# Optimization experiments

Measured on AMD Instinct MI355X. Metric: run time of the kernel, lower is better.

Reference implementation:

```python
import jax, jax.numpy as jnp
import numpy as np

EPS_COS = 1e-8   # torch cosine_similarity eps
EPS_LN = 1e-5    # torch LayerNorm eps
SLOPE = 0.01     # torch LeakyReLU default negative_slope
N_HOP = 3
D_MODEL = 512
TEMP = 10.0


def _cos_sim(q, s):
    # q: [B, D], s: [B, S, D] -> [B, S]
    dot = jnp.einsum('bd,bsd->bs', q, s)
    qn = jnp.linalg.norm(q, axis=-1)          # [B]
    sn = jnp.linalg.norm(s, axis=-1)          # [B, S]
    return dot / jnp.maximum(qn[:, None] * sn, EPS_COS)


def _layer_norm(x, gamma, beta):
    mu = jnp.mean(x, axis=-1, keepdims=True)
    var = jnp.mean(jnp.square(x - mu), axis=-1, keepdims=True)
    return (x - mu) * jax.lax.rsqrt(var + EPS_LN) * gamma + beta


def setup_inputs() -> dict:
    key = jax.random.key(0)
    k1, k2, k3, k4 = jax.random.split(key, 4)
    B, S, D = 256, 512, D_MODEL
    query_emb = jax.random.normal(k1, (B, D), dtype=jnp.float32)
    state_emb = jax.random.normal(k2, (B, S, D), dtype=jnp.float32)
    # Stacked per-hop Linear params (txt branch), kaiming-uniform-ish scale
    lim = 1.0 / np.sqrt(D)
    W = jax.random.uniform(k3, (N_HOP, D, D), jnp.float32, -lim, lim)
    b = jax.random.uniform(k4, (N_HOP, D), jnp.float32, -lim, lim)
    ln_gamma = jnp.ones((D,), jnp.float32)
    ln_beta = jnp.zeros((D,), jnp.float32)
    return {"query_emb": query_emb, "state_emb": state_emb, "W": W, "b": b,
            "ln_gamma": ln_gamma, "ln_beta": ln_beta}


def reference(query_emb, state_emb, W, b, ln_gamma, ln_beta):
    q, s = query_emb, state_emb
    for i in range(N_HOP):
        dist = jax.nn.softmax(_cos_sim(q, s) * TEMP, axis=-1)       # [B, S]
        s = jax.nn.leaky_relu(jnp.einsum('bsd,de->bse', s, W[i].T) + b[i],
                              negative_slope=SLOPE)                  # [B, S, D]
        agg = jnp.einsum('bs,bsd->bd', dist, s)                      # [B, D]
        q = _layer_norm(q + agg, ln_gamma, ln_beta)
    final_dist = jax.nn.softmax(_cos_sim(q, s) * TEMP, axis=-1)
    return (q, final_dist)
```

## Files before the change

### kernel.cpp

```cpp
#include <hip/hip_runtime.h>
#include <hip/hip_bf16.h>
#include <stdint.h>

#define D 512
#define BATCH 256
#define SEQ 512

typedef __attribute__((ext_vector_type(8))) short short8;
typedef __attribute__((ext_vector_type(4))) float floatx4;

__device__ __forceinline__ float bf2f(unsigned short u) {
    union { unsigned int i; float f; } x; x.i = ((unsigned int)u) << 16; return x.f;
}
__device__ __forceinline__ unsigned short f2bf(float f) {
    union { float f; unsigned int i; } x; x.f = f;
    unsigned int i = x.i;
    unsigned int lsb = (i >> 16) & 1u;
    i += 0x7fffu + lsb;
    return (unsigned short)(i >> 16);
}

__device__ __forceinline__ float wred_sum(float v) {
    #pragma unroll
    for (int o = 32; o; o >>= 1) v += __shfl_xor(v, o, 64);
    return v;
}

__device__ __forceinline__ void llds16(const void* g, void* l) {
    auto gp = (const __attribute__((address_space(1))) void*)(g);
    auto lp = (__attribute__((address_space(3))) void*)(uintptr_t)(l);
    __builtin_amdgcn_global_load_lds(gp, lp, 16, 0, 0);
}

#define FENCE() asm volatile("" ::: "memory")
#define BARRIER() do { FENCE(); __builtin_amdgcn_s_barrier(); FENCE(); } while (0)

template<int WN>
__device__ __forceinline__ void waitvm() {
    if constexpr (WN == 6)      asm volatile("s_waitcnt vmcnt(6)" ::: "memory");
    else if constexpr (WN == 4) asm volatile("s_waitcnt vmcnt(4)" ::: "memory");
    else if constexpr (WN == 2) asm volatile("s_waitcnt vmcnt(2)" ::: "memory");
    else if constexpr (WN == 0) asm volatile("s_waitcnt vmcnt(0)" ::: "memory");
}

template<bool F32IN>
__global__ __launch_bounds__(512)
void scores_kernel(const void* __restrict__ s_in_, const float* __restrict__ q,
                   float* __restrict__ dist_out, unsigned short* __restrict__ s_bf_out) {
    const int b = blockIdx.x, t = threadIdx.x, lane = t & 63, w = t >> 6;
    __shared__ float sc[SEQ];
    __shared__ float red[8];
    __shared__ float m_s, sum_s;

    float qv[8];
    {
        const float4* qp = (const float4*)(q + (size_t)b * D + lane * 8);
        float4 a = qp[0], c = qp[1];
        qv[0] = a.x; qv[1] = a.y; qv[2] = a.z; qv[3] = a.w;
        qv[4] = c.x; qv[5] = c.y; qv[6] = c.z; qv[7] = c.w;
    }
    float qn2 = 0.f;
    #pragma unroll
    for (int j = 0; j < 8; ++j) qn2 += qv[j] * qv[j];
    const float qn = sqrtf(wred_sum(qn2));

    const size_t bbase = (size_t)b * (SEQ * D);
    for (int j = 0; j < 64; j += 2) {
        const int r0 = w * 64 + j;
        float v0[8], v1[8];
        const size_t off0 = bbase + (size_t)r0 * D + lane * 8;
        const size_t off1 = off0 + D;
        if (F32IN) {
            const float4* p0 = (const float4*)((const float*)s_in_ + off0);
            const float4* p1 = (const float4*)((const float*)s_in_ + off1);
            float4 a0 = p0[0], c0 = p0[1], a1 = p1[0], c1 = p1[1];
            v0[0]=a0.x; v0[1]=a0.y; v0[2]=a0.z; v0[3]=a0.w;
            v0[4]=c0.x; v0[5]=c0.y; v0[6]=c0.z; v0[7]=c0.w;
            v1[0]=a1.x; v1[1]=a1.y; v1[2]=a1.z; v1[3]=a1.w;
            v1[4]=c1.x; v1[5]=c1.y; v1[6]=c1.z; v1[7]=c1.w;
            short8 w0, w1;
            #pragma unroll
            for (int k = 0; k < 8; ++k) { w0[k] = (short)f2bf(v0[k]); w1[k] = (short)f2bf(v1[k]); }
            *(short8*)(s_bf_out + off0) = w0;
            *(short8*)(s_bf_out + off1) = w1;
        } else {
            short8 w0 = *(const short8*)((const unsigned short*)s_in_ + off0);
            short8 w1 = *(const short8*)((const unsigned short*)s_in_ + off1);
            #pragma unroll
            for (int k = 0; k < 8; ++k) { v0[k] = bf2f((unsigned short)w0[k]); v1[k] = bf2f((unsigned short)w1[k]); }
        }
        float d0 = 0.f, n0 = 0.f, d1 = 0.f, n1 = 0.f;
        #pragma unroll
        for (int k = 0; k < 8; ++k) {
            d0 += v0[k] * qv[k]; n0 += v0[k] * v0[k];
            d1 += v1[k] * qv[k]; n1 += v1[k] * v1[k];
        }
        d0 = wred_sum(d0); n0 = wred_sum(n0);
        d1 = wred_sum(d1); n1 = wred_sum(n1);
        if (lane == 0) {
            sc[r0]     = 10.f * d0 / fmaxf(qn * sqrtf(n0), 1e-8f);
            sc[r0 + 1] = 10.f * d1 / fmaxf(qn * sqrtf(n1), 1e-8f);
        }
    }
    __syncthreads();

    const float sv = sc[t];
    float m = sv;
    #pragma unroll
    for (int o = 32; o; o >>= 1) m = fmaxf(m, __shfl_xor(m, o, 64));
    if (lane == 0) red[w] = m;
    __syncthreads();
    if (t == 0) {
        float mm = red[0];
        #pragma unroll
        for (int k = 1; k < 8; ++k) mm = fmaxf(mm, red[k]);
        m_s = mm;
    }
    __syncthreads();
    const float e = __expf(sv - m_s);
    float es = wred_sum(e);
    if (lane == 0) red[w] = es;
    __syncthreads();
    if (t == 0) {
        float s = 0.f;
        #pragma unroll
        for (int k = 0; k < 8; ++k) s += red[k];
        sum_s = s;
    }
    __syncthreads();
    dist_out[b * SEQ + t] = e / sum_s;
}

#define NKT 8

#define STA(BUF, H, KT) { const unsigned short* s_ = pA + (H) * 128 * D + (KT) * 64; \
    llds16(s_, &AsL[BUF][H][t * 8]); llds16(s_ + 64 * D, &AsL[BUF][H][t * 8 + 4096]); }
#define STB(BUF, H, KT) { const unsigned short* s_ = pB + (H) * 128 * D + (KT) * 64; \
    llds16(s_, &BsL[BUF][H][t * 8]); llds16(s_ + 64 * D, &BsL[BUF][H][t * 8 + 4096]); }

#define LDAF(BUF, MH) { _Pragma("unroll") for (int j = 0; j < 4; ++j) { \
    af[j][0] = *(const short8*)&AsL[BUF][MH][aoff[j] + xk0]; \
    af[j][1] = *(const short8*)&AsL[BUF][MH][aoff[j] + xk1]; } }
#define LDBF(BUF, NH) { _Pragma("unroll") for (int i = 0; i < 2; ++i) { \
    bfr[i][0] = *(const short8*)&BsL[BUF][NH][boff[i] + xk0]; \
    bfr[i][1] = *(const short8*)&BsL[BUF][NH][boff[i] + xk1]; } }

#define MMQ(MH, NH) { __builtin_amdgcn_s_setprio(1); \
    _Pragma("unroll") for (int kh = 0; kh < 2; ++kh) \
    _Pragma("unroll") for (int j = 0; j < 4; ++j) \
    _Pragma("unroll") for (int i = 0; i < 2; ++i) \
        acc[(MH) * 4 + j][(NH) * 2 + i] = __builtin_amdgcn_mfma_f32_16x16x32_bf16( \
            af[j][kh], bfr[i][kh], acc[(MH) * 4 + j][(NH) * 2 + i], 0, 0, 0); \
    __builtin_amdgcn_s_setprio(0); }

__global__ __launch_bounds__(512, 2)
void gemm_kernel(const unsigned short* __restrict__ A, const unsigned short* __restrict__ Bt,
                 const float* __restrict__ bias, const float* __restrict__ dist,
                 unsigned short* __restrict__ C, float* __restrict__ part) {
    __shared__ __align__(16) unsigned short AsL[2][2][128 * 64];
    __shared__ __align__(16) unsigned short BsL[2][2][128 * 64];
    __shared__ float dls[256];
    __shared__ float agg_lds[2][256];

    const int t = threadIdx.x, lane = t & 63, wid = t >> 6;
    const int wr = wid >> 2, wc = wid & 3;
    const int rr = lane & 15, lg = lane >> 4;
    const int mB = blockIdx.x >> 1, nB = blockIdx.x & 1;
    const size_t tileM = (size_t)mB * 256;
    const int tileN = nB * 256;

    float b_r[4];
    #pragma unroll
    for (int ni = 0; ni < 4; ++ni) b_r[ni] = bias[tileN + (ni * 4 + wc) * 16 + rr];

    if (t < 128) {
        float2 v = *(const float2*)&dist[tileM + 2 * t];
        dls[2 * t] = v.x; dls[2 * t + 1] = v.y;
    }
    asm volatile("s_waitcnt lgkmcnt(0)" ::: "memory");

    const int srow = t >> 3, gc = (t & 7) ^ (srow & 7);
    const unsigned short* pA = A + (tileM + srow) * D + gc * 8;
    const unsigned short* pB = Bt + (size_t)(tileN + srow) * D + gc * 8;

    int aoff[4], boff[2];
    #pragma unroll
    for (int j = 0; j < 4; ++j) aoff[j] = ((j * 2 + wr) * 16 + rr) * 64;
    #pragma unroll
    for (int i = 0; i < 2; ++i) boff[i] = ((i * 4 + wc) * 16 + rr) * 64;
    const int xk0 = ((lg) ^ (rr & 7)) * 8;
    const int xk1 = ((4 + lg) ^ (rr & 7)) * 8;

    floatx4 acc[8][4];
    #pragma unroll
    for (int i = 0; i < 8; ++i)
        #pragma unroll
        for (int j = 0; j < 4; ++j) acc[i][j] = {0.f, 0.f, 0.f, 0.f};

    short8 af[4][2], bfr[2][2];

    STA(0, 0, 0); STB(0, 0, 0); STB(0, 1, 0); STA(0, 1, 0);

    for (int kt = 0; kt < NKT - 1; ++kt) {
        const int rb = kt & 1, sb = rb ^ 1, nk = kt + 1;
        STA(sb, 0, nk); waitvm<6>(); BARRIER();
        LDAF(rb, 0); LDBF(rb, 0); MMQ(0, 0); BARRIER();
        STB(sb, 0, nk); waitvm<6>(); BARRIER();
        LDBF(rb, 1); MMQ(0, 1); BARRIER();
        STB(sb, 1, nk); waitvm<6>(); BARRIER();
        LDAF(rb, 1); LDBF(rb, 0); MMQ(1, 0); BARRIER();
        STA(sb, 1, nk); BARRIER();
        LDBF(rb, 1); MMQ(1, 1); BARRIER();
    }
    {
        waitvm<4>(); BARRIER();
        LDAF(1, 0); LDBF(1, 0); MMQ(0, 0); BARRIER();
        waitvm<2>(); BARRIER();
        LDBF(1, 1); MMQ(0, 1); BARRIER();
        waitvm<0>(); BARRIER();
        LDAF(1, 1); LDBF(1, 0); MMQ(1, 0); BARRIER();
        LDBF(1, 1); MMQ(1, 1);
    }
    __syncthreads();

    float pacc[4] = {0.f, 0.f, 0.f, 0.f};
    #pragma unroll
    for (int mi = 0; mi < 8; ++mi) {
        const int rowb = (mi * 2 + wr) * 16 + lg * 4;
        const float4 dv = *(const float4*)&dls[rowb];
        #pragma unroll
        for (int ni = 0; ni < 4; ++ni) {
            const int col = tileN + (ni * 4 + wc) * 16 + rr;
            #pragma unroll
            for (int r2 = 0; r2 < 4; ++r2) {
                float v = acc[mi][ni][r2] + b_r[ni];
                v = v >= 0.f ? v : 0.01f * v;
                C[(tileM + rowb + r2) * D + col] = f2bf(v);
                pacc[ni] += (&dv.x)[r2] * v;
            }
        }
    }
    #pragma unroll
    for (int ni = 0; ni < 4; ++ni) {
        float p = pacc[ni];
        p += __shfl_xor(p, 16, 64);
        p += __shfl_xor(p, 32, 64);
        if (lg == 0) agg_lds[wr][(ni * 4 + wc) * 16 + rr] = p;
    }
    __syncthreads();
    if (t < 256) {
        const int b = mB >> 1;
        const float s = agg_lds[0][t] + agg_lds[1][t];
        part[(size_t)(mB & 1) * (BATCH * D) + (size_t)b * D + tileN + t] = s;
    }
}

__global__ __launch_bounds__(256)
void aggln_kernel(const float* __restrict__ part, const float* __restrict__ q_in,
                  const float* __restrict__ gamma, const float* __restrict__ beta,
                  float* __restrict__ q_out) {
    const int b = blockIdx.x, t = threadIdx.x, lane = t & 63, wv = t >> 6;
    __shared__ float red[8];
    __shared__ float mu_s, rstd_s;

    const int c0 = 2 * t;
    float2 v0 = *(const float2*)(part + (size_t)b * D + c0);
    float2 v1 = *(const float2*)(part + (size_t)(BATCH * D) + (size_t)b * D + c0);
    float x0 = q_in[b * D + c0] + v0.x + v1.x;
    float x1 = q_in[b * D + c0 + 1] + v0.y + v1.y;

    float sm = wred_sum(x0 + x1);
    if (lane == 0) red[wv] = sm;
    __syncthreads();
    if (t == 0) mu_s = (red[0] + red[1] + red[2] + red[3]) * (1.f / 512.f);
    __syncthreads();
    const float mu = mu_s;
    float d0 = x0 - mu, d1 = x1 - mu;
    float vv = wred_sum(d0 * d0 + d1 * d1);
    if (lane == 0) red[wv] = vv;
    __syncthreads();
    if (t == 0) rstd_s = rsqrtf((red[0] + red[1] + red[2] + red[3]) * (1.f / 512.f) + 1e-5f);
    __syncthreads();
    const float rs = rstd_s;
    q_out[b * D + c0]     = d0 * rs * gamma[c0]     + beta[c0];
    q_out[b * D + c0 + 1] = d1 * rs * gamma[c0 + 1] + beta[c0 + 1];
}

__global__ __launch_bounds__(256)
void convw_kernel(const float* __restrict__ W, unsigned short* __restrict__ Wb, int n4) {
    int i = blockIdx.x * 256 + threadIdx.x;
    if (i < n4) {
        float4 v = *(const float4*)(W + (size_t)i * 4);
        ushort4 o;
        o.x = f2bf(v.x); o.y = f2bf(v.y); o.z = f2bf(v.z); o.w = f2bf(v.w);
        *(ushort4*)(Wb + (size_t)i * 4) = o;
    }
}

extern "C" void kernel_launch(void* const* d_in, const int* in_sizes, int n_in,
                              void* d_out, int out_size, void* d_ws, size_t ws_size,
                              hipStream_t stream) {
    const float* query = (const float*)d_in[0];
    const float* state = (const float*)d_in[1];
    const float* W     = (const float*)d_in[2];
    const float* bias  = (const float*)d_in[3];
    const float* gamma = (const float*)d_in[4];
    const float* beta  = (const float*)d_in[5];

    float* out_q    = (float*)d_out;
    float* out_dist = (float*)d_out + BATCH * SEQ;

    char* ws = (char*)d_ws;
    const size_t SBYTES = (size_t)BATCH * SEQ * D * 2;
    unsigned short* sA = (unsigned short*)ws;
    unsigned short* sB = (unsigned short*)(ws + SBYTES);
    char* ext = ws + 2 * SBYTES;
    float* dist = (float*)ext;
    float* qbuf = (float*)(ext + 524288);
    float* part = (float*)(ext + 2 * 524288);
    unsigned short* Wb = (unsigned short*)(ext + 4 * 524288);

    hipMemcpyAsync(qbuf, query, (size_t)BATCH * D * sizeof(float),
                   hipMemcpyDeviceToDevice, stream);
    convw_kernel<<<768, 256, 0, stream>>>(W, Wb, 3 * D * D / 4);

    dim3 ggrid(BATCH * SEQ / 256 * 2);

    scores_kernel<true><<<BATCH, 512, 0, stream>>>(state, qbuf, dist, sA);
    gemm_kernel<<<ggrid, 512, 0, stream>>>(sA, Wb, bias, dist, sB, part);
    aggln_kernel<<<BATCH, 256, 0, stream>>>(part, qbuf, gamma, beta, qbuf);
    scores_kernel<false><<<BATCH, 512, 0, stream>>>(sB, qbuf, dist, nullptr);
    gemm_kernel<<<ggrid, 512, 0, stream>>>(sB, Wb + D * D, bias + D, dist, sA, part);
    aggln_kernel<<<BATCH, 256, 0, stream>>>(part, qbuf, gamma, beta, qbuf);
    scores_kernel<false><<<BATCH, 512, 0, stream>>>(sA, qbuf, dist, nullptr);
    gemm_kernel<<<ggrid, 512, 0, stream>>>(sA, Wb + 2 * D * D, bias + 2 * D, dist, sB, part);
    aggln_kernel<<<BATCH, 256, 0, stream>>>(part, qbuf, gamma, beta, out_q);
    scores_kernel<false><<<BATCH, 512, 0, stream>>>(sB, out_q, out_dist, nullptr);
}
```

Baseline: 489.8 us.

## Fuse LayerNorm into cosine-score softmax kernel and widen score blocks to 1024 threads

Merges the aggregate+LayerNorm kernel into the following cosine-similarity/softmax kernel, so the updated query is computed in LDS and scored in one launch. It also drops the initial query memcpy by reading the input query directly. Score kernels now use 1024 threads, with 16-lane groups per row covering the full row in 4 strided chunks, which gives more rows in flight and shorter reductions. The trade-off is fewer launches and less q round-tripping against larger blocks with idle half-threads during the softmax phase.

```diff
diff --git a/kernel.cpp b/kernel.cpp
--- a/kernel.cpp
+++ b/kernel.cpp
@@ -25,6 +25,11 @@
     for (int o = 32; o; o >>= 1) v += __shfl_xor(v, o, 64);
     return v;
 }
+__device__ __forceinline__ float gred_sum16(float v) {
+    #pragma unroll
+    for (int o = 8; o; o >>= 1) v += __shfl_xor(v, o, 64);
+    return v;
+}
 
 __device__ __forceinline__ void llds16(const void* g, void* l) {
     auto gp = (const __attribute__((address_space(1))) void*)(g);
@@ -43,72 +48,66 @@
     else if constexpr (WN == 0) asm volatile("s_waitcnt vmcnt(0)" ::: "memory");
 }
 
-template<bool F32IN>
-__global__ __launch_bounds__(512)
-void scores_kernel(const void* __restrict__ s_in_, const float* __restrict__ q,
-                   float* __restrict__ dist_out, unsigned short* __restrict__ s_bf_out) {
+__global__ __launch_bounds__(1024)
+void scores0_kernel(const float* __restrict__ state, const float* __restrict__ query,
+                    float* __restrict__ dist_out, unsigned short* __restrict__ s_bf_out) {
     const int b = blockIdx.x, t = threadIdx.x, lane = t & 63, w = t >> 6;
+    const int g = lane >> 4, ll = lane & 15;
     __shared__ float sc[SEQ];
     __shared__ float red[8];
     __shared__ float m_s, sum_s;
 
-    float qv[8];
+    float qv[4][8];
     {
-        const float4* qp = (const float4*)(q + (size_t)b * D + lane * 8);
-        float4 a = qp[0], c = qp[1];
-        qv[0] = a.x; qv[1] = a.y; qv[2] = a.z; qv[3] = a.w;
-        qv[4] = c.x; qv[5] = c.y; qv[6] = c.z; qv[7] = c.w;
+        const float* qp = query + (size_t)b * D + ll * 8;
+        #pragma unroll
+        for (int j = 0; j < 4; ++j) {
+            float4 a = *(const float4*)(qp + j * 128);
+            float4 c = *(const float4*)(qp + j * 128 + 4);
+            qv[j][0]=a.x; qv[j][1]=a.y; qv[j][2]=a.z; qv[j][3]=a.w;
+            qv[j][4]=c.x; qv[j][5]=c.y; qv[j][6]=c.z; qv[j][7]=c.w;
+        }
     }
     float qn2 = 0.f;
     #pragma unroll
-    for (int j = 0; j < 8; ++j) qn2 += qv[j] * qv[j];
-    const float qn = sqrtf(wred_sum(qn2));
+    for (int j = 0; j < 4; ++j)
+        #pragma unroll
+        for (int e = 0; e < 8; ++e) qn2 += qv[j][e] * qv[j][e];
+    const float qn = sqrtf(gred_sum16(qn2));
 
     const size_t bbase = (size_t)b * (SEQ * D);
-    for (int j = 0; j < 64; j += 2) {
-        const int r0 = w * 64 + j;
-        float v0[8], v1[8];
-        const size_t off0 = bbase + (size_t)r0 * D + lane * 8;
-        const size_t off1 = off0 + D;
-        if (F32IN) {
-            const float4* p0 = (const float4*)((const float*)s_in_ + off0);
-            const float4* p1 = (const float4*)((const float*)s_in_ + off1);
-            float4 a0 = p0[0], c0 = p0[1], a1 = p1[0], c1 = p1[1];
-            v0[0]=a0.x; v0[1]=a0.y; v0[2]=a0.z; v0[3]=a0.w;
-            v0[4]=c0.x; v0[5]=c0.y; v0[6]=c0.z; v0[7]=c0.w;
-            v1[0]=a1.x; v1[1]=a1.y; v1[2]=a1.z; v1[3]=a1.w;
-            v1[4]=c1.x; v1[5]=c1.y; v1[6]=c1.z; v1[7]=c1.w;
-            short8 w0, w1;
+    #pragma unroll 2
+    for (int i = 0; i < 8; ++i) {
+        const int row = w * 32 + i * 4 + g;
+        const float* rp = state + bbase + (size_t)row * D + ll * 8;
+        unsigned short* op = s_bf_out + bbase + (size_t)row * D + ll * 8;
+        float dot = 0.f, nr = 0.f;
+        #pragma unroll
+        for (int j = 0; j < 4; ++j) {
+            float4 a = *(const float4*)(rp + j * 128);
+            float4 c = *(const float4*)(rp + j * 128 + 4);
+            float v[8] = {a.x, a.y, a.z, a.w, c.x, c.y, c.z, c.w};
+            short8 wv;
             #pragma unroll
-            for (int k = 0; k < 8; ++k) { w0[k] = (short)f2bf(v0[k]); w1[k] = (short)f2bf(v1[k]); }
-            *(short8*)(s_bf_out + off0) = w0;
-            *(short8*)(s_bf_out + off1) = w1;
-        } else {
-            short8 w0 = *(const short8*)((const unsigned short*)s_in_ + off0);
-            short8 w1 = *(const short8*)((const unsigned short*)s_in_ + off1);
+            for (int e = 0; e < 8; ++e) wv[e] = (short)f2bf(v[e]);
+            *(short8*)(op + j * 128) = wv;
             #pragma unroll
-            for (int k = 0; k < 8; ++k) { v0[k] = bf2f((unsigned short)w0[k]); v1[k] = bf2f((unsigned short)w1[k]); }
+            for (int e = 0; e < 8; ++e) { dot += v[e] * qv[j][e]; nr += v[e] * v[e]; }
         }
-        float d0 = 0.f, n0 = 0.f, d1 = 0.f, n1 = 0.f;
-        #pragma unroll
-        for (int k = 0; k < 8; ++k) {
-            d0 += v0[k] * qv[k]; n0 += v0[k] * v0[k];
-            d1 += v1[k] * qv[k]; n1 += v1[k] * v1[k];
-        }
-        d0 = wred_sum(d0); n0 = wred_sum(n0);
-        d1 = wred_sum(d1); n1 = wred_sum(n1);
-        if (lane == 0) {
-            sc[r0]     = 10.f * d0 / fmaxf(qn * sqrtf(n0), 1e-8f);
-            sc[r0 + 1] = 10.f * d1 / fmaxf(qn * sqrtf(n1), 1e-8f);
-        }
-    }
-    __syncthreads();
-
-    const float sv = sc[t];
-    float m = sv;
-    #pragma unroll
-    for (int o = 32; o; o >>= 1) m = fmaxf(m, __shfl_xor(m, o, 64));
-    if (lane == 0) red[w] = m;
+        dot = gred_sum16(dot);
+        nr  = gred_sum16(nr);
+        if (ll == 0) sc[row] = 10.f * dot / fmaxf(qn * sqrtf(nr), 1e-8f);
+    }
+    __syncthreads();
+
+    float sv = 0.f, ev = 0.f;
+    if (t < 512) {
+        sv = sc[t];
+        float m = sv;
+        #pragma unroll
+        for (int o = 32; o; o >>= 1) m = fmaxf(m, __shfl_xor(m, o, 64));
+        if (lane == 0) red[w] = m;
+    }
     __syncthreads();
     if (t == 0) {
         float mm = red[0];
@@ -117,9 +116,11 @@
         m_s = mm;
     }
     __syncthreads();
-    const float e = __expf(sv - m_s);
-    float es = wred_sum(e);
-    if (lane == 0) red[w] = es;
+    if (t < 512) {
+        ev = __expf(sv - m_s);
+        float es = wred_sum(ev);
+        if (lane == 0) red[w] = es;
+    }
     __syncthreads();
     if (t == 0) {
         float s = 0.f;
@@ -128,7 +129,111 @@
         sum_s = s;
     }
     __syncthreads();
-    dist_out[b * SEQ + t] = e / sum_s;
+    if (t < 512) dist_out[b * SEQ + t] = ev / sum_s;
+}
+
+__global__ __launch_bounds__(1024)
+void fused_kernel(const unsigned short* __restrict__ S, const float* __restrict__ part,
+                  const float* __restrict__ q_in, const float* __restrict__ gamma,
+                  const float* __restrict__ beta, float* __restrict__ q_out,
+                  float* __restrict__ dist_out) {
+    const int b = blockIdx.x, t = threadIdx.x, lane = t & 63, w = t >> 6;
+    const int g = lane >> 4, ll = lane & 15;
+    __shared__ float qs[D];
+    __shared__ float sc[SEQ];
+    __shared__ float red[8];
+    __shared__ float mu_s, rstd_s, qn_s, m_s, sum_s;
+
+    float x = 0.f;
+    if (t < 512) {
+        const float a = part[(size_t)b * D + t] + part[(size_t)(BATCH * D) + (size_t)b * D + t];
+        x = q_in[(size_t)b * D + t] + a;
+        float sm = wred_sum(x);
+        if (lane == 0) red[w] = sm;
+    }
+    __syncthreads();
+    if (t == 0) mu_s = (red[0]+red[1]+red[2]+red[3]+red[4]+red[5]+red[6]+red[7]) * (1.f / 512.f);
+    __syncthreads();
+    if (t < 512) {
+        const float d = x - mu_s;
+        float vv = wred_sum(d * d);
+        if (lane == 0) red[w] = vv;
+    }
+    __syncthreads();
+    if (t == 0) rstd_s = rsqrtf((red[0]+red[1]+red[2]+red[3]+red[4]+red[5]+red[6]+red[7]) * (1.f / 512.f) + 1e-5f);
+    __syncthreads();
+    if (t < 512) {
+        const float y = (x - mu_s) * rstd_s * gamma[t] + beta[t];
+        q_out[(size_t)b * D + t] = y;
+        qs[t] = y;
+        float s2 = wred_sum(y * y);
+        if (lane == 0) red[w] = s2;
+    }
+    __syncthreads();
+    if (t == 0) qn_s = sqrtf(red[0]+red[1]+red[2]+red[3]+red[4]+red[5]+red[6]+red[7]);
+    __syncthreads();
+
+    float qv[4][8];
+    #pragma unroll
+    for (int j = 0; j < 4; ++j) {
+        float4 a = *(const float4*)&qs[j * 128 + ll * 8];
+        float4 c = *(const float4*)&qs[j * 128 + ll * 8 + 4];
+        qv[j][0]=a.x; qv[j][1]=a.y; qv[j][2]=a.z; qv[j][3]=a.w;
+        qv[j][4]=c.x; qv[j][5]=c.y; qv[j][6]=c.z; qv[j][7]=c.w;
+    }
+    const float qn = qn_s;
+    const size_t bbase = (size_t)b * (SEQ * D);
+    #pragma unroll 2
+    for (int i = 0; i < 8; ++i) {
+        const int row = w * 32 + i * 4 + g;
+        const unsigned short* rp = S + bbase + (size_t)row * D + ll * 8;
+        float dot = 0.f, nr = 0.f;
+        #pragma unroll
+        for (int j = 0; j < 4; ++j) {
+            short8 wv = *(const short8*)(rp + j * 128);
+            #pragma unroll
+            for (int e = 0; e < 8; ++e) {
+                const float v = bf2f((unsigned short)wv[e]);
+                dot += v * qv[j][e];
+                nr += v * v;
+            }
+        }
+        dot = gred_sum16(dot);
+        nr  = gred_sum16(nr);
+        if (ll == 0) sc[row] = 10.f * dot / fmaxf(qn * sqrtf(nr), 1e-8f);
+    }
+    __syncthreads();
+
+    float sv = 0.f, ev = 0.f;
+    if (t < 512) {
+        sv = sc[t];
+        float m = sv;
+        #pragma unroll
+        for (int o = 32; o; o >>= 1) m = fmaxf(m, __shfl_xor(m, o, 64));
+        if (lane == 0) red[w] = m;
+    }
+    __syncthreads();
+    if (t == 0) {
+        float mm = red[0];
+        #pragma unroll
+        for (int k = 1; k < 8; ++k) mm = fmaxf(mm, red[k]);
+        m_s = mm;
+    }
+    __syncthreads();
+    if (t < 512) {
+        ev = __expf(sv - m_s);
+        float es = wred_sum(ev);
+        if (lane == 0) red[w] = es;
+    }
+    __syncthreads();
+    if (t == 0) {
+        float s = 0.f;
+        #pragma unroll
+        for (int k = 0; k < 8; ++k) s += red[k];
+        sum_s = s;
+    }
+    __syncthreads();
+    if (t < 512) dist_out[b * SEQ + t] = ev / sum_s;
 }
 
 #define NKT 8
@@ -256,37 +361,6 @@
 }
 
 __global__ __launch_bounds__(256)
-void aggln_kernel(const float* __restrict__ part, const float* __restrict__ q_in,
-                  const float* __restrict__ gamma, const float* __restrict__ beta,
-                  float* __restrict__ q_out) {
-    const int b = blockIdx.x, t = threadIdx.x, lane = t & 63, wv = t >> 6;
-    __shared__ float red[8];
-    __shared__ float mu_s, rstd_s;
-
-    const int c0 = 2 * t;
-    float2 v0 = *(const float2*)(part + (size_t)b * D + c0);
-    float2 v1 = *(const float2*)(part + (size_t)(BATCH * D) + (size_t)b * D + c0);
-    float x0 = q_in[b * D + c0] + v0.x + v1.x;
-    float x1 = q_in[b * D + c0 + 1] + v0.y + v1.y;
-
-    float sm = wred_sum(x0 + x1);
-    if (lane == 0) red[wv] = sm;
-    __syncthreads();
-    if (t == 0) mu_s = (red[0] + red[1] + red[2] + red[3]) * (1.f / 512.f);
-    __syncthreads();
-    const float mu = mu_s;
-    float d0 = x0 - mu, d1 = x1 - mu;
-    float vv = wred_sum(d0 * d0 + d1 * d1);
-    if (lane == 0) red[wv] = vv;
-    __syncthreads();
-    if (t == 0) rstd_s = rsqrtf((red[0] + red[1] + red[2] + red[3]) * (1.f / 512.f) + 1e-5f);
-    __syncthreads();
-    const float rs = rstd_s;
-    q_out[b * D + c0]     = d0 * rs * gamma[c0]     + beta[c0];
-    q_out[b * D + c0 + 1] = d1 * rs * gamma[c0 + 1] + beta[c0 + 1];
-}
-
-__global__ __launch_bounds__(256)
 void convw_kernel(const float* __restrict__ W, unsigned short* __restrict__ Wb, int n4) {
     int i = blockIdx.x * 256 + threadIdx.x;
     if (i < n4) {
@@ -320,20 +394,15 @@
     float* part = (float*)(ext + 2 * 524288);
     unsigned short* Wb = (unsigned short*)(ext + 4 * 524288);
 
-    hipMemcpyAsync(qbuf, query, (size_t)BATCH * D * sizeof(float),
-                   hipMemcpyDeviceToDevice, stream);
     convw_kernel<<<768, 256, 0, stream>>>(W, Wb, 3 * D * D / 4);
 
     dim3 ggrid(BATCH * SEQ / 256 * 2);
 
-    scores_kernel<true><<<BATCH, 512, 0, stream>>>(state, qbuf, dist, sA);
+    scores0_kernel<<<BATCH, 1024, 0, stream>>>(state, query, dist, sA);
     gemm_kernel<<<ggrid, 512, 0, stream>>>(sA, Wb, bias, dist, sB, part);
-    aggln_kernel<<<BATCH, 256, 0, stream>>>(part, qbuf, gamma, beta, qbuf);
-    scores_kernel<false><<<BATCH, 512, 0, stream>>>(sB, qbuf, dist, nullptr);
+    fused_kernel<<<BATCH, 1024, 0, stream>>>(sB, part, query, gamma, beta, qbuf, dist);
     gemm_kernel<<<ggrid, 512, 0, stream>>>(sB, Wb + D * D, bias + D, dist, sA, part);
-    aggln_kernel<<<BATCH, 256, 0, stream>>>(part, qbuf, gamma, beta, qbuf);
-    scores_kernel<false><<<BATCH, 512, 0, stream>>>(sA, qbuf, dist, nullptr);
+    fused_kernel<<<BATCH, 1024, 0, stream>>>(sA, part, qbuf, gamma, beta, qbuf, dist);
     gemm_kernel<<<ggrid, 512, 0, stream>>>(sA, Wb + 2 * D * D, bias + 2 * D, dist, sB, part);
-    aggln_kernel<<<BATCH, 256, 0, stream>>>(part, qbuf, gamma, beta, out_q);
-    scores_kernel<false><<<BATCH, 512, 0, stream>>>(sB, out_q, out_dist, nullptr);
-}
+    fused_kernel<<<BATCH, 1024, 0, stream>>>(sB, part, qbuf, gamma, beta, out_q, out_dist);
+}
```

After: 439.0 us. -10.4%, faster.
